# Optimization experiments

Hardware: AMD Instinct MI355X
Metric: run time of the kernel (lower is better)

Reference implementation:

```python
import jax, jax.numpy as jnp
import numpy as np

N_NODES = 50000
N_EDGES = 800000
IN_DIM = 128
HIDDEN = 128
OUT_DIM = 128


def setup_inputs() -> dict:
    key = jax.random.key(0)
    ks = jax.random.split(key, 16)
    s = 0.05
    inp = {
        "x": jax.random.normal(ks[0], (N_NODES, IN_DIM), jnp.float32),
        "edge_index": jax.random.randint(ks[1], (2, N_EDGES), 0, N_NODES, jnp.int64),
        "batch": jax.random.randint(ks[2], (25000,), 0, N_NODES, jnp.int64),
        "labels": jax.random.randint(ks[3], (N_NODES,), 0, 2, jnp.int64),
        # SAGEConv layer 1: in->hidden
        "W1l": jax.random.normal(ks[4], (HIDDEN, IN_DIM), jnp.float32) * s,
        "b1": jnp.zeros((HIDDEN,), jnp.float32),
        "W1r": jax.random.normal(ks[5], (HIDDEN, IN_DIM), jnp.float32) * s,
        # SAGEConv layer 2: hidden->hidden
        "W2l": jax.random.normal(ks[6], (HIDDEN, HIDDEN), jnp.float32) * s,
        "b2": jnp.zeros((HIDDEN,), jnp.float32),
        "W2r": jax.random.normal(ks[7], (HIDDEN, HIDDEN), jnp.float32) * s,
        # SAGEConv layer 3: hidden->out
        "W3l": jax.random.normal(ks[8], (OUT_DIM, HIDDEN), jnp.float32) * s,
        "b3": jnp.zeros((OUT_DIM,), jnp.float32),
        "W3r": jax.random.normal(ks[9], (OUT_DIM, HIDDEN), jnp.float32) * s,
        # classifier head: out->2
        "Wlin": jax.random.normal(ks[10], (2, OUT_DIM), jnp.float32) * s,
        "blin": jnp.zeros((2,), jnp.float32),
    }
    return inp


def _sage_conv(h, src, dst, Wl, bl, Wr):
    # mean aggregation of source features at destination nodes
    msg = h[src]                                            # [E, d]
    ssum = jax.ops.segment_sum(msg, dst, num_segments=N_NODES)
    cnt = jax.ops.segment_sum(jnp.ones((src.shape[0], 1), h.dtype), dst,
                              num_segments=N_NODES)
    agg = ssum / jnp.maximum(cnt, 1.0)
    # lin_l(agg) + lin_r(h): aggregate-then-transform (same math, cheaper)
    return agg @ Wl.T + bl + h @ Wr.T


def reference(x, edge_index, batch, labels,
              W1l, b1, W1r, W2l, b2, W2r, W3l, b3, W3r, Wlin, blin):
    src, dst = edge_index[0], edge_index[1]
    h = jax.nn.relu(_sage_conv(x, src, dst, W1l, b1, W1r))
    h = jax.nn.relu(_sage_conv(h, src, dst, W2l, b2, W2r))
    h = _sage_conv(h, src, dst, W3l, b3, W3r)               # no act after last
    preds = jax.nn.softmax(h @ Wlin.T + blin, axis=1)       # nn.Softmax(dim=1)
    # CrossEntropyLoss on (already-softmaxed) preds, as in the original module
    logp = jax.nn.log_softmax(preds[batch], axis=1)
    loss = -jnp.mean(jnp.take_along_axis(logp, labels[batch][:, None], axis=1))
    return loss
```

## Files before the change

### kernel.cpp

```cpp
#include <hip/hip_runtime.h>
#include <hip/hip_bf16.h>

#define N_NODES 50000
#define MPAD    50048
#define N_EDGES 800000
#define DIM     128
#define N_BATCH 25000
#define NBUCK   196
#define BCAP    8192
#define NBIN    64

typedef unsigned short u16;
typedef unsigned int   u32;
typedef unsigned char  u8;
typedef unsigned long long u64;

typedef __attribute__((ext_vector_type(8))) short bf16x8;
typedef __attribute__((ext_vector_type(4))) float f32x4;

static __device__ __forceinline__ float bf2f(u16 u) {
    union { u32 i; float f; } v; v.i = ((u32)u) << 16; return v.f;
}
static __device__ __forceinline__ u16 f2bf(float f) {
    union { float f; u32 i; } v; v.f = f;
    u32 x = v.i;
    u32 r = x + 0x7fffu + ((x >> 16) & 1u);
    return (u16)(r >> 16);
}


__global__ void k_init(int* bcur, float* accum, int* hcount,
                       u8* mask, int* h1g, int* h3g) {
    int gid = blockIdx.x * 256 + threadIdx.x;
    if (gid < NBUCK) bcur[gid] = gid * BCAP;
    if (gid < NBIN) { h1g[gid] = 0; h3g[gid] = 0; }
    if (gid < N_NODES) mask[gid] = 0;
    if (gid == 0) { accum[0] = 0.f; hcount[0] = 0; }
}

__global__ void k_mark(const int* __restrict__ batch, u8* __restrict__ mask) {
    int s = blockIdx.x * 256 + threadIdx.x;
    if (s < N_BATCH) mask[batch[s]] = 1;
}


__global__ __launch_bounds__(256) void k_part(const int* __restrict__ src,
                                              const int* __restrict__ dst,
                                              int* __restrict__ bcur,
                                              u64* __restrict__ ebuf) {
    __shared__ int hist[NBUCK];
    __shared__ int lbase[NBUCK];
    __shared__ int gdelta[NBUCK];
    __shared__ u64 stage[4096];
    __shared__ int gaddr[4096];
    int t = threadIdx.x;
    for (int i = t; i < NBUCK; i += 256) hist[i] = 0;
    __syncthreads();

    int base = blockIdx.x * 4096;
    int cnt = N_EDGES - base; if (cnt > 4096) cnt = 4096; if (cnt < 0) cnt = 0;

    int es[16], ed[16], rr[16];
#pragma unroll
    for (int k = 0; k < 16; ++k) {
        int i = t + (k << 8);
        bool ok = i < cnt;
        int e = ok ? (base + i) : 0;
        int s = src[e], d = dst[e];
        es[k] = s; ed[k] = d;
        int r = -1;
        if (ok) r = atomicAdd(&hist[d >> 8], 1);
        rr[k] = r;
    }
    __syncthreads();

    if (t < 64) {
        int run = 0;
        for (int c = 0; c < 4; ++c) {
            int idx = c * 64 + t;
            int v = (idx < NBUCK) ? hist[idx] : 0;
            int orig = v;
            for (int off = 1; off < 64; off <<= 1) {
                int u = __shfl_up(v, off);
                if (t >= off) v += u;
            }
            int tot = __shfl(v, 63);
            if (idx < NBUCK) lbase[idx] = run + v - orig;
            run += tot;
        }
    }
    __syncthreads();

    if (t < NBUCK) {
        int c = hist[t];
        int g = atomicAdd(&bcur[t], c);
        gdelta[t] = g - lbase[t];
    }
    __syncthreads();

#pragma unroll
    for (int k = 0; k < 16; ++k) {
        if (rr[k] >= 0) {
            int b = ed[k] >> 8;
            int slot = lbase[b] + rr[k];
            stage[slot] = (((u64)(u32)ed[k]) << 32) | (u32)es[k];
            gaddr[slot] = gdelta[b] + slot;
        }
    }
    __syncthreads();

    for (int i = t; i < cnt; i += 256) {
        ebuf[gaddr[i]] = stage[i];
    }
}


__global__ void k_bscan(const int* __restrict__ bcur, int* __restrict__ bbase) {
    int t = threadIdx.x;
    int run = 0;
    for (int c = 0; c < 4; ++c) {
        int idx = c * 64 + t;
        int v = (idx < NBUCK) ? (bcur[idx] - idx * BCAP) : 0;
        int orig = v;
        for (int off = 1; off < 64; off <<= 1) {
            int u = __shfl_up(v, off);
            if (t >= off) v += u;
        }
        int tot = __shfl(v, 63);
        if (idx < NBUCK) bbase[idx] = run + v - orig;
        run += tot;
    }
}


__global__ __launch_bounds__(256) void k_build(const u64* __restrict__ ebuf,
                                               const int* __restrict__ bcur,
                                               const int* __restrict__ bbase,
                                               const u8* __restrict__ mask,
                                               int* __restrict__ row_ptr,
                                               int* __restrict__ deg,
                                               float* __restrict__ deg_inv,
                                               int* __restrict__ csr_src,
                                               int* __restrict__ h1g,
                                               int* __restrict__ h3g) {
    __shared__ int cnt256[256];
    __shared__ int sh[256];
    __shared__ int cur[256];
    __shared__ int bh1[NBIN];
    __shared__ int bh3[NBIN];
    int b  = blockIdx.x;
    int t  = threadIdx.x;
    int n0 = b << 8;
    cnt256[t] = 0;
    if (t < NBIN) { bh1[t] = 0; bh3[t] = 0; }
    __syncthreads();

    int cnt = bcur[b] - b * BCAP;
    const u64* eb = ebuf + (size_t)b * BCAP;
    for (int i = t; i < cnt; i += 256) {
        int d = (int)(eb[i] >> 32);
        atomicAdd(&cnt256[d - n0], 1);
    }
    __syncthreads();

    int myc = cnt256[t];
    sh[t] = myc;
    __syncthreads();
    for (int off = 1; off < 256; off <<= 1) {
        int x = (t >= off) ? sh[t - off] : 0;
        __syncthreads();
        sh[t] += x;
        __syncthreads();
    }
    int rp = bbase[b] + sh[t] - myc;
    int n  = n0 + t;
    if (n < N_NODES) {
        row_ptr[n] = rp;
        deg[n]     = myc;
        deg_inv[n] = 1.0f / (float)(myc < 1 ? 1 : myc);
        int bin = myc < NBIN ? myc : NBIN - 1;
        atomicAdd(&bh1[bin], 1);
        if (mask[n]) atomicAdd(&bh3[bin], 1);
    }
    cur[t] = rp;
    __syncthreads();

    for (int i = t; i < cnt; i += 256) {
        u64 p = eb[i];
        int d = (int)(p >> 32);
        int s = (int)(u32)p;
        int pos = atomicAdd(&cur[d - n0], 1);
        csr_src[pos] = s;
    }
    __syncthreads();
    if (t < NBIN) {
        if (bh1[t]) atomicAdd(&h1g[t], bh1[t]);
        if (bh3[t]) atomicAdd(&h3g[t], bh3[t]);
    }
}


__global__ void k_dscan(int* __restrict__ h1g, int* __restrict__ h3g,
                        int* __restrict__ n3out) {
    int t = threadIdx.x;
    int v1 = h1g[t], v3 = h3g[t];
    int o1 = v1, o3 = v3;
    for (int off = 1; off < 64; off <<= 1) {
        int u1 = __shfl_up(v1, off);
        int u3 = __shfl_up(v3, off);
        if (t >= off) { v1 += u1; v3 += u3; }
    }
    if (t == 63) n3out[0] = v3;
    h1g[t] = v1 - o1;
    h3g[t] = v3 - o3;
}


__global__ __launch_bounds__(256) void k_dscatter(const int* __restrict__ deg,
                                                  const u8* __restrict__ mask,
                                                  int* __restrict__ h1g,
                                                  int* __restrict__ h3g,
                                                  int* __restrict__ wl1,
                                                  int* __restrict__ wl3) {
    __shared__ int bh1[NBIN], bh3[NBIN], bb1[NBIN], bb3[NBIN];
    int t = threadIdx.x;
    int n = blockIdx.x * 256 + t;
    if (t < NBIN) { bh1[t] = 0; bh3[t] = 0; }
    __syncthreads();
    bool valid = n < N_NODES;
    int d = 0, r1 = -1, r3 = -1;
    if (valid) {
        d = deg[n]; if (d >= NBIN) d = NBIN - 1;
        r1 = atomicAdd(&bh1[d], 1);
        if (mask[n]) r3 = atomicAdd(&bh3[d], 1);
    }
    __syncthreads();
    if (t < NBIN) {
        bb1[t] = atomicAdd(&h1g[t], bh1[t]);
        bb3[t] = atomicAdd(&h3g[t], bh3[t]);
    }
    __syncthreads();
    if (valid) {
        wl1[bb1[d] + r1] = n;
        if (r3 >= 0) wl3[bb3[d] + r3] = n;
    }
}


__global__ void k_cast_x(const float* __restrict__ x, u16* __restrict__ xb) {
    int gid = blockIdx.x * 256 + threadIdx.x;
    int row = gid >> 4;
    int c8  = (gid & 15) << 3;
    u32 outw[4];
    if (row < N_NODES) {
        const float4* p = (const float4*)(x + (size_t)row * DIM + c8);
        float4 v0 = p[0], v1 = p[1];
        outw[0] = (u32)f2bf(v0.x) | ((u32)f2bf(v0.y) << 16);
        outw[1] = (u32)f2bf(v0.z) | ((u32)f2bf(v0.w) << 16);
        outw[2] = (u32)f2bf(v1.x) | ((u32)f2bf(v1.y) << 16);
        outw[3] = (u32)f2bf(v1.z) | ((u32)f2bf(v1.w) << 16);
    } else {
        outw[0] = outw[1] = outw[2] = outw[3] = 0;
    }
    *(uint4*)(xb + (size_t)row * DIM + c8) = *(uint4*)outw;
}

__global__ void k_cast_w(const float* __restrict__ W1l, const float* __restrict__ W1r,
                         const float* __restrict__ W2l, const float* __restrict__ W2r,
                         const float* __restrict__ W3l, const float* __restrict__ W3r,
                         u16* __restrict__ out) {
    int i = blockIdx.x * 256 + threadIdx.x;
    int mat = i >> 14, off = i & 16383;
    const float* src = (mat == 0) ? W1l : (mat == 1) ? W1r : (mat == 2) ? W2l
                     : (mat == 3) ? W2r : (mat == 4) ? W3l : W3r;
    out[i] = f2bf(src[off]);
}


template <bool RELU, bool PRUNED>
__global__ __launch_bounds__(256) void k_sage(
    const u16* __restrict__ h, const int* __restrict__ csr_src,
    const int* __restrict__ row_ptr, const int* __restrict__ deg,
    const float* __restrict__ deg_inv,
    const int* __restrict__ wl, const int* __restrict__ wlN,
    const u16* __restrict__ Wl, const u16* __restrict__ Wr,
    const float* __restrict__ bias, u16* __restrict__ out) {
    __shared__ u16 tile[16 * 128];
    __shared__ int wlid[16];
    int nwl = PRUNED ? wlN[0] : N_NODES;
    int m0  = blockIdx.x * 16;
    if (m0 >= nwl) return;

    int t    = threadIdx.x;
    int lane = t & 63;
    int wid  = t >> 6;
    int sub  = lane & 15;
    int grp  = lane >> 4;
    int nloc = (wid << 2) + grp;
    int gb   = lane & 48;
    int node = (m0 + nloc < nwl) ? wl[m0 + nloc] : -1;
    if (sub == 0) wlid[nloc] = node;

    float a0 = 0, a1 = 0, a2 = 0, a3 = 0, a4 = 0, a5 = 0, a6 = 0, a7 = 0;

#define ACC(u) { a0 += bf2f((u16)((u).x & 0xffffu)); a1 += bf2f((u16)((u).x >> 16)); \
                 a2 += bf2f((u16)((u).y & 0xffffu)); a3 += bf2f((u16)((u).y >> 16)); \
                 a4 += bf2f((u16)((u).z & 0xffffu)); a5 += bf2f((u16)((u).z >> 16)); \
                 a6 += bf2f((u16)((u).w & 0xffffu)); a7 += bf2f((u16)((u).w >> 16)); }

    if (node >= 0) {
        int start = row_ptr[node];
        int cnt   = deg[node];
        for (int c0 = 0; c0 < cnt; c0 += 16) {
            int rem = cnt - c0; if (rem > 16) rem = 16;
            int sidx = 0;
            if (sub < rem) sidx = csr_src[start + c0 + sub];
            int j = 0;
            for (; j + 8 <= rem; j += 8) {
                int i0 = __shfl(sidx, gb + j);
                int i1 = __shfl(sidx, gb + j + 1);
                int i2 = __shfl(sidx, gb + j + 2);
                int i3 = __shfl(sidx, gb + j + 3);
                int i4 = __shfl(sidx, gb + j + 4);
                int i5 = __shfl(sidx, gb + j + 5);
                int i6 = __shfl(sidx, gb + j + 6);
                int i7 = __shfl(sidx, gb + j + 7);
                uint4 r0 = *(const uint4*)(h + (size_t)i0 * DIM + sub * 8);
                uint4 r1 = *(const uint4*)(h + (size_t)i1 * DIM + sub * 8);
                uint4 r2 = *(const uint4*)(h + (size_t)i2 * DIM + sub * 8);
                uint4 r3 = *(const uint4*)(h + (size_t)i3 * DIM + sub * 8);
                uint4 r4 = *(const uint4*)(h + (size_t)i4 * DIM + sub * 8);
                uint4 r5 = *(const uint4*)(h + (size_t)i5 * DIM + sub * 8);
                uint4 r6 = *(const uint4*)(h + (size_t)i6 * DIM + sub * 8);
                uint4 r7 = *(const uint4*)(h + (size_t)i7 * DIM + sub * 8);
                ACC(r0); ACC(r1); ACC(r2); ACC(r3);
                ACC(r4); ACC(r5); ACC(r6); ACC(r7);
            }
            for (; j + 4 <= rem; j += 4) {
                int i0 = __shfl(sidx, gb + j);
                int i1 = __shfl(sidx, gb + j + 1);
                int i2 = __shfl(sidx, gb + j + 2);
                int i3 = __shfl(sidx, gb + j + 3);
                uint4 r0 = *(const uint4*)(h + (size_t)i0 * DIM + sub * 8);
                uint4 r1 = *(const uint4*)(h + (size_t)i1 * DIM + sub * 8);
                uint4 r2 = *(const uint4*)(h + (size_t)i2 * DIM + sub * 8);
                uint4 r3 = *(const uint4*)(h + (size_t)i3 * DIM + sub * 8);
                ACC(r0); ACC(r1); ACC(r2); ACC(r3);
            }
            for (; j < rem; ++j) {
                int i0 = __shfl(sidx, gb + j);
                uint4 r0 = *(const uint4*)(h + (size_t)i0 * DIM + sub * 8);
                ACC(r0);
            }
        }
        float inv = deg_inv[node];
        a0 *= inv; a1 *= inv; a2 *= inv; a3 *= inv;
        a4 *= inv; a5 *= inv; a6 *= inv; a7 *= inv;
    }
#undef ACC

    {
        uint4 o;
        o.x = (u32)f2bf(a0) | ((u32)f2bf(a1) << 16);
        o.y = (u32)f2bf(a2) | ((u32)f2bf(a3) << 16);
        o.z = (u32)f2bf(a4) | ((u32)f2bf(a5) << 16);
        o.w = (u32)f2bf(a6) | ((u32)f2bf(a7) << 16);
        int chunk = sub ^ (nloc & 7);
        *(uint4*)&tile[nloc * 128 + chunk * 8] = o;
    }
    __syncthreads();

    const int fr = sub;
    const int kq = grp << 3;
    bf16x8 aF0[4], aF1[4];
    int rnode = wlid[fr];
    int safe_r = rnode < 0 ? 0 : rnode;
    const u16* ph = h + (size_t)safe_r * DIM + kq;
#pragma unroll
    for (int kt = 0; kt < 4; ++kt) {
        int c = (grp + kt * 4) ^ (fr & 7);
        aF0[kt] = *(const bf16x8*)&tile[fr * 128 + c * 8];
        aF1[kt] = *(const bf16x8*)(ph + kt * 32);
    }
#pragma unroll
    for (int q = 0; q < 2; ++q) {
        int nt = wid * 2 + q;
        const u16* pwl = Wl + (size_t)(nt * 16 + fr) * DIM + kq;
        const u16* pwr = Wr + (size_t)(nt * 16 + fr) * DIM + kq;
        f32x4 acc = {0.f, 0.f, 0.f, 0.f};
#pragma unroll
        for (int kt = 0; kt < 4; ++kt) {
            bf16x8 w = *(const bf16x8*)(pwl + kt * 32);
            acc = __builtin_amdgcn_mfma_f32_16x16x32_bf16(aF0[kt], w, acc, 0, 0, 0);
        }
#pragma unroll
        for (int kt = 0; kt < 4; ++kt) {
            bf16x8 w = *(const bf16x8*)(pwr + kt * 32);
            acc = __builtin_amdgcn_mfma_f32_16x16x32_bf16(aF1[kt], w, acc, 0, 0, 0);
        }
        int col = nt * 16 + fr;
        float b = bias[col];
#pragma unroll
        for (int j = 0; j < 4; ++j) {
            int onode = wlid[(grp << 2) + j];
            if (onode >= 0) {
                float v = acc[j] + b;
                if (RELU) v = fmaxf(v, 0.f);
                out[(size_t)onode * DIM + col] = f2bf(v);
            }
        }
    }
}


__global__ __launch_bounds__(256) void k_head(
    const u16* __restrict__ h3, const int* __restrict__ batch,
    const int* __restrict__ labels, const float* __restrict__ Wlin,
    const float* __restrict__ blin, float* __restrict__ accum,
    int* __restrict__ hcount, float* __restrict__ out) {
    __shared__ float wsh[256];
    __shared__ float red[4];
    int t = threadIdx.x;
    wsh[t] = Wlin[t];
    __syncthreads();

    int lane = t & 63;
    int g    = lane >> 4;
    int sub  = lane & 15;
    int wv   = (blockIdx.x * 256 + t) >> 6;
    int samp = wv * 4 + g;

    float contrib = 0.f;
    float z0 = 0.f, z1 = 0.f;
    int n = 0;
    if (samp < N_BATCH) {
        n = batch[samp];
        uint4 u = *(const uint4*)(h3 + (size_t)n * DIM + sub * 8);
        const u32* uw = (const u32*)&u;
        int cb = sub * 8;
#pragma unroll
        for (int q = 0; q < 4; ++q) {
            float hlo = bf2f((u16)(uw[q] & 0xffffu));
            float hhi = bf2f((u16)(uw[q] >> 16));
            z0 += hlo * wsh[cb + q * 2]       + hhi * wsh[cb + q * 2 + 1];
            z1 += hlo * wsh[128 + cb + q * 2] + hhi * wsh[128 + cb + q * 2 + 1];
        }
    }
#pragma unroll
    for (int off = 8; off > 0; off >>= 1) {
        z0 += __shfl_xor(z0, off);
        z1 += __shfl_xor(z1, off);
    }
    if (samp < N_BATCH) {
        z0 += blin[0]; z1 += blin[1];
        float m  = fmaxf(z0, z1);
        float e0 = expf(z0 - m), e1 = expf(z1 - m);
        float s  = e0 + e1;
        float p0 = e0 / s, p1 = e1 / s;
        float m2  = fmaxf(p0, p1);
        float lse = m2 + logf(expf(p0 - m2) + expf(p1 - m2));
        int lab = labels[n];
        float lp = ((lab == 0) ? p0 : p1) - lse;
        if (sub == 0) contrib = -lp * (1.0f / (float)N_BATCH);
    }
#pragma unroll
    for (int off = 16; off < 64; off <<= 1) contrib += __shfl_xor(contrib, off);
    if (lane == 0) red[t >> 6] = contrib;
    __syncthreads();
    if (t == 0) {
        atomicAdd(accum, red[0] + red[1] + red[2] + red[3]);
        __threadfence();
        int c = atomicAdd(hcount, 1);
        if (c == (int)gridDim.x - 1) {
            float v = atomicAdd(accum, 0.0f);
            out[0] = v;
        }
    }
}


extern "C" void kernel_launch(void* const* d_in, const int* in_sizes, int n_in,
                              void* d_out, int out_size, void* d_ws, size_t ws_size,
                              hipStream_t stream) {
    const float* x    = (const float*)d_in[0];
    const int*   eidx = (const int*)d_in[1];
    const int*   batch  = (const int*)d_in[2];
    const int*   labels = (const int*)d_in[3];
    const float* W1l = (const float*)d_in[4];
    const float* b1  = (const float*)d_in[5];
    const float* W1r = (const float*)d_in[6];
    const float* W2l = (const float*)d_in[7];
    const float* b2  = (const float*)d_in[8];
    const float* W2r = (const float*)d_in[9];
    const float* W3l = (const float*)d_in[10];
    const float* b3  = (const float*)d_in[11];
    const float* W3r = (const float*)d_in[12];
    const float* Wlin = (const float*)d_in[13];
    const float* blin = (const float*)d_in[14];

    const int* src = eidx;
    const int* dst = eidx + N_EDGES;

    size_t off = 0;
    auto alloc = [&](size_t bytes) -> char* {
        off = (off + 511) & ~(size_t)511;
        char* p = (char*)d_ws + off;
        off += bytes;
        return p;
    };
    int*   bcur    = (int*)  alloc(NBUCK * 4);
    int*   bbase   = (int*)  alloc(NBUCK * 4);
    int*   row_ptr = (int*)  alloc(N_NODES * 4);
    int*   deg     = (int*)  alloc(N_NODES * 4);
    float* deg_inv = (float*)alloc(N_NODES * 4);
    int*   csr_src = (int*)  alloc(N_EDGES * 4);
    u64*   ebuf    = (u64*)  alloc((size_t)NBUCK * BCAP * 8);
    u16*   wb      = (u16*)  alloc(6 * DIM * DIM * 2);
    u16*   xb      = (u16*)  alloc((size_t)MPAD * DIM * 2);
    u16*   bufA    = (u16*)  alloc((size_t)MPAD * DIM * 2);
    u8*    mask    = (u8*)   alloc(N_NODES);
    int*   h1g     = (int*)  alloc(NBIN * 4);
    int*   h3g     = (int*)  alloc(NBIN * 4);
    int*   wl1     = (int*)  alloc(MPAD * 4);
    int*   wl3     = (int*)  alloc(MPAD * 4);
    int*   n3      = (int*)  alloc(4);
    float* accum   = (float*)alloc(4);
    int*   hcount  = (int*)  alloc(4);

    u16* bufB = xb;

    u16* w1l = wb + 0 * DIM * DIM;
    u16* w1r = wb + 1 * DIM * DIM;
    u16* w2l = wb + 2 * DIM * DIM;
    u16* w2r = wb + 3 * DIM * DIM;
    u16* w3l = wb + 4 * DIM * DIM;
    u16* w3r = wb + 5 * DIM * DIM;

    const int NB196 = (N_NODES + 255) / 256;
    const int PB    = (N_EDGES + 4095) / 4096;
    const int MB    = (N_BATCH + 255) / 256;
    const int CXB   = MPAD * 16 / 256;
    const int CWB   = 6 * DIM * DIM / 256;
    const int SGB   = N_NODES / 16;
    const int HB2   = (N_BATCH + 15) / 16;

    k_init<<<NB196, 256, 0, stream>>>(bcur, accum, hcount, mask, h1g, h3g);
    k_part<<<PB, 256, 0, stream>>>(src, dst, bcur, ebuf);
    k_bscan<<<1, 64, 0, stream>>>(bcur, bbase);
    k_mark<<<MB, 256, 0, stream>>>(batch, mask);
    k_build<<<NBUCK, 256, 0, stream>>>(ebuf, bcur, bbase, mask, row_ptr, deg,
                                       deg_inv, csr_src, h1g, h3g);
    k_dscan<<<1, 64, 0, stream>>>(h1g, h3g, n3);
    k_dscatter<<<NB196, 256, 0, stream>>>(deg, mask, h1g, h3g, wl1, wl3);

    k_cast_x<<<CXB, 256, 0, stream>>>(x, xb);
    k_cast_w<<<CWB, 256, 0, stream>>>(W1l, W1r, W2l, W2r, W3l, W3r, wb);

    k_sage<true, false><<<SGB, 256, 0, stream>>>(xb, csr_src, row_ptr, deg, deg_inv,
                                                 wl1, n3, w1l, w1r, b1, bufA);
    k_sage<true, false><<<SGB, 256, 0, stream>>>(bufA, csr_src, row_ptr, deg, deg_inv,
                                                 wl1, n3, w2l, w2r, b2, bufB);
    k_sage<false, true><<<SGB, 256, 0, stream>>>(bufB, csr_src, row_ptr, deg, deg_inv,
                                                 wl3, n3, w3l, w3r, b3, bufA);

    k_head<<<HB2, 256, 0, stream>>>(bufA, batch, labels, Wlin, blin,
                                    accum, hcount, (float*)d_out);
}
```

Before: 218.7 us.

## Gather neighbor features in FP8 and fuse setup kernels to cut launches

Measured after the change: 191.1 us (median of 2 runs). -12.6%, faster.

```diff
diff --git a/kernel.cpp b/kernel.cpp
--- a/kernel.cpp
+++ b/kernel.cpp
@@ -17,6 +17,7 @@
 
 typedef __attribute__((ext_vector_type(8))) short bf16x8;
 typedef __attribute__((ext_vector_type(4))) float f32x4;
+typedef __attribute__((ext_vector_type(2))) float f32x2;
 
 static __device__ __forceinline__ float bf2f(u16 u) {
     union { u32 i; float f; } v; v.i = ((u32)u) << 16; return v.f;
@@ -27,133 +28,166 @@
     u32 r = x + 0x7fffu + ((x >> 16) & 1u);
     return (u16)(r >> 16);
 }
-
-
-__global__ void k_init(int* bcur, float* accum, int* hcount,
-                       u8* mask, int* h1g, int* h3g) {
+template <bool HI>
+static __device__ __forceinline__ u32 pk8(float a, float b, u32 old) {
+    return (u32)__builtin_amdgcn_cvt_pk_fp8_f32(a, b, (int)old, HI);
+}
+
+
+__global__ void k_init(int* bcur, float* accum, int* hcount, u8* mask,
+                       int* c1g, int* c3g, int* o1g, int* o3g) {
     int gid = blockIdx.x * 256 + threadIdx.x;
     if (gid < NBUCK) bcur[gid] = gid * BCAP;
-    if (gid < NBIN) { h1g[gid] = 0; h3g[gid] = 0; }
+    if (gid < NBIN) { c1g[gid] = 0; c3g[gid] = 0; o1g[gid] = 0; o3g[gid] = 0; }
     if (gid < N_NODES) mask[gid] = 0;
     if (gid == 0) { accum[0] = 0.f; hcount[0] = 0; }
 }
 
-__global__ void k_mark(const int* __restrict__ batch, u8* __restrict__ mask) {
-    int s = blockIdx.x * 256 + threadIdx.x;
-    if (s < N_BATCH) mask[batch[s]] = 1;
-}
-
-
-__global__ __launch_bounds__(256) void k_part(const int* __restrict__ src,
-                                              const int* __restrict__ dst,
-                                              int* __restrict__ bcur,
-                                              u64* __restrict__ ebuf) {
+
+#define SB_PART 196
+#define SB_CX   3324
+#define SB_CW   3708
+#define SB_MK   3806
+
+__global__ __launch_bounds__(256) void k_setup(
+    const int* __restrict__ src, const int* __restrict__ dst,
+    int* __restrict__ bcur, u64* __restrict__ ebuf,
+    const float* __restrict__ x, u16* __restrict__ xb, u8* __restrict__ x8,
+    const float* __restrict__ W1l, const float* __restrict__ W1r,
+    const float* __restrict__ W2l, const float* __restrict__ W2r,
+    const float* __restrict__ W3l, const float* __restrict__ W3r,
+    u16* __restrict__ wout,
+    const int* __restrict__ batch, u8* __restrict__ mask) {
     __shared__ int hist[NBUCK];
     __shared__ int lbase[NBUCK];
     __shared__ int gdelta[NBUCK];
     __shared__ u64 stage[4096];
     __shared__ int gaddr[4096];
+    int bid = blockIdx.x;
     int t = threadIdx.x;
-    for (int i = t; i < NBUCK; i += 256) hist[i] = 0;
-    __syncthreads();
-
-    int base = blockIdx.x * 4096;
-    int cnt = N_EDGES - base; if (cnt > 4096) cnt = 4096; if (cnt < 0) cnt = 0;
-
-    int es[16], ed[16], rr[16];
-#pragma unroll
-    for (int k = 0; k < 16; ++k) {
-        int i = t + (k << 8);
-        bool ok = i < cnt;
-        int e = ok ? (base + i) : 0;
-        int s = src[e], d = dst[e];
-        es[k] = s; ed[k] = d;
-        int r = -1;
-        if (ok) r = atomicAdd(&hist[d >> 8], 1);
-        rr[k] = r;
-    }
-    __syncthreads();
-
-    if (t < 64) {
-        int run = 0;
-        for (int c = 0; c < 4; ++c) {
-            int idx = c * 64 + t;
-            int v = (idx < NBUCK) ? hist[idx] : 0;
-            int orig = v;
-            for (int off = 1; off < 64; off <<= 1) {
-                int u = __shfl_up(v, off);
-                if (t >= off) v += u;
+
+    if (bid < SB_PART) {
+        for (int i = t; i < NBUCK; i += 256) hist[i] = 0;
+        __syncthreads();
+
+        int base = bid * 4096;
+        int cnt = N_EDGES - base; if (cnt > 4096) cnt = 4096; if (cnt < 0) cnt = 0;
+
+        int es[16], ed[16], rr[16];
+#pragma unroll
+        for (int k = 0; k < 16; ++k) {
+            int i = t + (k << 8);
+            bool ok = i < cnt;
+            int e = ok ? (base + i) : 0;
+            int s = src[e], d = dst[e];
+            es[k] = s; ed[k] = d;
+            int r = -1;
+            if (ok) r = atomicAdd(&hist[d >> 8], 1);
+            rr[k] = r;
+        }
+        __syncthreads();
+
+        if (t < 64) {
+            int run = 0;
+            for (int c = 0; c < 4; ++c) {
+                int idx = c * 64 + t;
+                int v = (idx < NBUCK) ? hist[idx] : 0;
+                int orig = v;
+                for (int off = 1; off < 64; off <<= 1) {
+                    int u = __shfl_up(v, off);
+                    if (t >= off) v += u;
+                }
+                int tot = __shfl(v, 63);
+                if (idx < NBUCK) lbase[idx] = run + v - orig;
+                run += tot;
             }
-            int tot = __shfl(v, 63);
-            if (idx < NBUCK) lbase[idx] = run + v - orig;
-            run += tot;
-        }
-    }
-    __syncthreads();
-
-    if (t < NBUCK) {
-        int c = hist[t];
-        int g = atomicAdd(&bcur[t], c);
-        gdelta[t] = g - lbase[t];
-    }
-    __syncthreads();
-
-#pragma unroll
-    for (int k = 0; k < 16; ++k) {
-        if (rr[k] >= 0) {
-            int b = ed[k] >> 8;
-            int slot = lbase[b] + rr[k];
-            stage[slot] = (((u64)(u32)ed[k]) << 32) | (u32)es[k];
-            gaddr[slot] = gdelta[b] + slot;
-        }
-    }
-    __syncthreads();
-
-    for (int i = t; i < cnt; i += 256) {
-        ebuf[gaddr[i]] = stage[i];
-    }
-}
-
-
-__global__ void k_bscan(const int* __restrict__ bcur, int* __restrict__ bbase) {
-    int t = threadIdx.x;
-    int run = 0;
-    for (int c = 0; c < 4; ++c) {
-        int idx = c * 64 + t;
-        int v = (idx < NBUCK) ? (bcur[idx] - idx * BCAP) : 0;
-        int orig = v;
-        for (int off = 1; off < 64; off <<= 1) {
-            int u = __shfl_up(v, off);
-            if (t >= off) v += u;
-        }
-        int tot = __shfl(v, 63);
-        if (idx < NBUCK) bbase[idx] = run + v - orig;
-        run += tot;
+        }
+        __syncthreads();
+
+        if (t < NBUCK) {
+            int c = hist[t];
+            int g = atomicAdd(&bcur[t], c);
+            gdelta[t] = g - lbase[t];
+        }
+        __syncthreads();
+
+#pragma unroll
+        for (int k = 0; k < 16; ++k) {
+            if (rr[k] >= 0) {
+                int b = ed[k] >> 8;
+                int slot = lbase[b] + rr[k];
+                stage[slot] = (((u64)(u32)ed[k]) << 32) | (u32)es[k];
+                gaddr[slot] = gdelta[b] + slot;
+            }
+        }
+        __syncthreads();
+
+        for (int i = t; i < cnt; i += 256) {
+            ebuf[gaddr[i]] = stage[i];
+        }
+    } else if (bid < SB_CX) {
+        int gid = (bid - SB_PART) * 256 + t;
+        int row = gid >> 4;
+        int c8  = (gid & 15) << 3;
+        u32 outw[4];
+        u32 w0 = 0, w1 = 0;
+        if (row < N_NODES) {
+            const float4* p = (const float4*)(x + (size_t)row * DIM + c8);
+            float4 v0 = p[0], v1 = p[1];
+            outw[0] = (u32)f2bf(v0.x) | ((u32)f2bf(v0.y) << 16);
+            outw[1] = (u32)f2bf(v0.z) | ((u32)f2bf(v0.w) << 16);
+            outw[2] = (u32)f2bf(v1.x) | ((u32)f2bf(v1.y) << 16);
+            outw[3] = (u32)f2bf(v1.z) | ((u32)f2bf(v1.w) << 16);
+            w0 = pk8<false>(v0.x, v0.y, 0); w0 = pk8<true>(v0.z, v0.w, w0);
+            w1 = pk8<false>(v1.x, v1.y, 0); w1 = pk8<true>(v1.z, v1.w, w1);
+        } else {
+            outw[0] = outw[1] = outw[2] = outw[3] = 0;
+        }
+        *(uint4*)(xb + (size_t)row * DIM + c8) = *(uint4*)outw;
+        uint2 o8; o8.x = w0; o8.y = w1;
+        *(uint2*)(x8 + (size_t)row * DIM + c8) = o8;
+    } else if (bid < SB_CW) {
+        int i = (bid - SB_CX) * 256 + t;
+        int mat = i >> 14, off = i & 16383;
+        const float* s = (mat == 0) ? W1l : (mat == 1) ? W1r : (mat == 2) ? W2l
+                       : (mat == 3) ? W2r : (mat == 4) ? W3l : W3r;
+        wout[i] = f2bf(s[off]);
+    } else {
+        int s = (bid - SB_CW) * 256 + t;
+        if (s < N_BATCH) mask[batch[s]] = 1;
     }
 }
 
 
 __global__ __launch_bounds__(256) void k_build(const u64* __restrict__ ebuf,
                                                const int* __restrict__ bcur,
-                                               const int* __restrict__ bbase,
                                                const u8* __restrict__ mask,
                                                int* __restrict__ row_ptr,
                                                int* __restrict__ deg,
                                                float* __restrict__ deg_inv,
                                                int* __restrict__ csr_src,
-                                               int* __restrict__ h1g,
-                                               int* __restrict__ h3g) {
+                                               int* __restrict__ c1g,
+                                               int* __restrict__ c3g) {
     __shared__ int cnt256[256];
     __shared__ int sh[256];
     __shared__ int cur[256];
     __shared__ int bh1[NBIN];
     __shared__ int bh3[NBIN];
+    __shared__ int shbase;
     int b  = blockIdx.x;
     int t  = threadIdx.x;
     int n0 = b << 8;
     cnt256[t] = 0;
     if (t < NBIN) { bh1[t] = 0; bh3[t] = 0; }
-    __syncthreads();
+    if (t < 64) {
+        int s = 0;
+        for (int i = t; i < b; i += 64) s += bcur[i] - i * BCAP;
+#pragma unroll
+        for (int off = 32; off > 0; off >>= 1) s += __shfl_xor(s, off);
+        if (t == 0) shbase = s;
+    }
+    __syncthreads();
+    int bbase = shbase;
 
     int cnt = bcur[b] - b * BCAP;
     const u64* eb = ebuf + (size_t)b * BCAP;
@@ -172,7 +206,7 @@
         sh[t] += x;
         __syncthreads();
     }
-    int rp = bbase[b] + sh[t] - myc;
+    int rp = bbase + sh[t] - myc;
     int n  = n0 + t;
     if (n < N_NODES) {
         row_ptr[n] = rp;
@@ -194,34 +228,21 @@
     }
     __syncthreads();
     if (t < NBIN) {
-        if (bh1[t]) atomicAdd(&h1g[t], bh1[t]);
-        if (bh3[t]) atomicAdd(&h3g[t], bh3[t]);
-    }
-}
-
-
-__global__ void k_dscan(int* __restrict__ h1g, int* __restrict__ h3g,
-                        int* __restrict__ n3out) {
-    int t = threadIdx.x;
-    int v1 = h1g[t], v3 = h3g[t];
-    int o1 = v1, o3 = v3;
-    for (int off = 1; off < 64; off <<= 1) {
-        int u1 = __shfl_up(v1, off);
-        int u3 = __shfl_up(v3, off);
-        if (t >= off) { v1 += u1; v3 += u3; }
-    }
-    if (t == 63) n3out[0] = v3;
-    h1g[t] = v1 - o1;
-    h3g[t] = v3 - o3;
+        if (bh1[t]) atomicAdd(&c1g[t], bh1[t]);
+        if (bh3[t]) atomicAdd(&c3g[t], bh3[t]);
+    }
 }
 
 
 __global__ __launch_bounds__(256) void k_dscatter(const int* __restrict__ deg,
                                                   const u8* __restrict__ mask,
-                                                  int* __restrict__ h1g,
-                                                  int* __restrict__ h3g,
+                                                  const int* __restrict__ c1g,
+                                                  const int* __restrict__ c3g,
+                                                  int* __restrict__ o1g,
+                                                  int* __restrict__ o3g,
                                                   int* __restrict__ wl1,
-                                                  int* __restrict__ wl3) {
+                                                  int* __restrict__ wl3,
+                                                  int* __restrict__ n3) {
     __shared__ int bh1[NBIN], bh3[NBIN], bb1[NBIN], bb3[NBIN];
     int t = threadIdx.x;
     int n = blockIdx.x * 256 + t;
@@ -235,9 +256,19 @@
         if (mask[n]) r3 = atomicAdd(&bh3[d], 1);
     }
     __syncthreads();
-    if (t < NBIN) {
-        bb1[t] = atomicAdd(&h1g[t], bh1[t]);
-        bb3[t] = atomicAdd(&h3g[t], bh3[t]);
+    if (t < 64) {
+        int v1 = c1g[t], v3 = c3g[t];
+        int i1 = v1, i3 = v3;
+        for (int off = 1; off < 64; off <<= 1) {
+            int u1 = __shfl_up(i1, off);
+            int u3 = __shfl_up(i3, off);
+            if (t >= off) { i1 += u1; i3 += u3; }
+        }
+        int res1 = atomicAdd(&o1g[t], bh1[t]);
+        int res3 = atomicAdd(&o3g[t], bh3[t]);
+        bb1[t] = (i1 - v1) + res1;
+        bb3[t] = (i3 - v3) + res3;
+        if (blockIdx.x == 0 && t == 63) n3[0] = i3;
     }
     __syncthreads();
     if (valid) {
@@ -247,44 +278,16 @@
 }
 
 
-__global__ void k_cast_x(const float* __restrict__ x, u16* __restrict__ xb) {
-    int gid = blockIdx.x * 256 + threadIdx.x;
-    int row = gid >> 4;
-    int c8  = (gid & 15) << 3;
-    u32 outw[4];
-    if (row < N_NODES) {
-        const float4* p = (const float4*)(x + (size_t)row * DIM + c8);
-        float4 v0 = p[0], v1 = p[1];
-        outw[0] = (u32)f2bf(v0.x) | ((u32)f2bf(v0.y) << 16);
-        outw[1] = (u32)f2bf(v0.z) | ((u32)f2bf(v0.w) << 16);
-        outw[2] = (u32)f2bf(v1.x) | ((u32)f2bf(v1.y) << 16);
-        outw[3] = (u32)f2bf(v1.z) | ((u32)f2bf(v1.w) << 16);
-    } else {
-        outw[0] = outw[1] = outw[2] = outw[3] = 0;
-    }
-    *(uint4*)(xb + (size_t)row * DIM + c8) = *(uint4*)outw;
-}
-
-__global__ void k_cast_w(const float* __restrict__ W1l, const float* __restrict__ W1r,
-                         const float* __restrict__ W2l, const float* __restrict__ W2r,
-                         const float* __restrict__ W3l, const float* __restrict__ W3r,
-                         u16* __restrict__ out) {
-    int i = blockIdx.x * 256 + threadIdx.x;
-    int mat = i >> 14, off = i & 16383;
-    const float* src = (mat == 0) ? W1l : (mat == 1) ? W1r : (mat == 2) ? W2l
-                     : (mat == 3) ? W2r : (mat == 4) ? W3l : W3r;
-    out[i] = f2bf(src[off]);
-}
-
-
-template <bool RELU, bool PRUNED>
+template <bool RELU, bool PRUNED, bool W8>
 __global__ __launch_bounds__(256) void k_sage(
-    const u16* __restrict__ h, const int* __restrict__ csr_src,
+    const u16* __restrict__ h, const u8* __restrict__ h8,
+    const int* __restrict__ csr_src,
     const int* __restrict__ row_ptr, const int* __restrict__ deg,
     const float* __restrict__ deg_inv,
     const int* __restrict__ wl, const int* __restrict__ wlN,
     const u16* __restrict__ Wl, const u16* __restrict__ Wr,
-    const float* __restrict__ bias, u16* __restrict__ out) {
+    const float* __restrict__ bias, u16* __restrict__ out,
+    u8* __restrict__ out8) {
     __shared__ u16 tile[16 * 128];
     __shared__ int wlid[16];
     int nwl = PRUNED ? wlN[0] : N_NODES;
@@ -303,10 +306,11 @@
 
     float a0 = 0, a1 = 0, a2 = 0, a3 = 0, a4 = 0, a5 = 0, a6 = 0, a7 = 0;
 
-#define ACC(u) { a0 += bf2f((u16)((u).x & 0xffffu)); a1 += bf2f((u16)((u).x >> 16)); \
-                 a2 += bf2f((u16)((u).y & 0xffffu)); a3 += bf2f((u16)((u).y >> 16)); \
-                 a4 += bf2f((u16)((u).z & 0xffffu)); a5 += bf2f((u16)((u).z >> 16)); \
-                 a6 += bf2f((u16)((u).w & 0xffffu)); a7 += bf2f((u16)((u).w >> 16)); }
+#define ACC8(r) { f32x2 p; \
+    p = __builtin_amdgcn_cvt_pk_f32_fp8((r).x, false); a0 += p[0]; a1 += p[1]; \
+    p = __builtin_amdgcn_cvt_pk_f32_fp8((r).x, true);  a2 += p[0]; a3 += p[1]; \
+    p = __builtin_amdgcn_cvt_pk_f32_fp8((r).y, false); a4 += p[0]; a5 += p[1]; \
+    p = __builtin_amdgcn_cvt_pk_f32_fp8((r).y, true);  a6 += p[0]; a7 += p[1]; }
 
     if (node >= 0) {
         int start = row_ptr[node];
@@ -325,39 +329,39 @@
                 int i5 = __shfl(sidx, gb + j + 5);
                 int i6 = __shfl(sidx, gb + j + 6);
                 int i7 = __shfl(sidx, gb + j + 7);
-                uint4 r0 = *(const uint4*)(h + (size_t)i0 * DIM + sub * 8);
-                uint4 r1 = *(const uint4*)(h + (size_t)i1 * DIM + sub * 8);
-                uint4 r2 = *(const uint4*)(h + (size_t)i2 * DIM + sub * 8);
-                uint4 r3 = *(const uint4*)(h + (size_t)i3 * DIM + sub * 8);
-                uint4 r4 = *(const uint4*)(h + (size_t)i4 * DIM + sub * 8);
-                uint4 r5 = *(const uint4*)(h + (size_t)i5 * DIM + sub * 8);
-                uint4 r6 = *(const uint4*)(h + (size_t)i6 * DIM + sub * 8);
-                uint4 r7 = *(const uint4*)(h + (size_t)i7 * DIM + sub * 8);
-                ACC(r0); ACC(r1); ACC(r2); ACC(r3);
-                ACC(r4); ACC(r5); ACC(r6); ACC(r7);
+                uint2 r0 = *(const uint2*)(h8 + (size_t)i0 * DIM + sub * 8);
+                uint2 r1 = *(const uint2*)(h8 + (size_t)i1 * DIM + sub * 8);
+                uint2 r2 = *(const uint2*)(h8 + (size_t)i2 * DIM + sub * 8);
+                uint2 r3 = *(const uint2*)(h8 + (size_t)i3 * DIM + sub * 8);
+                uint2 r4 = *(const uint2*)(h8 + (size_t)i4 * DIM + sub * 8);
+                uint2 r5 = *(const uint2*)(h8 + (size_t)i5 * DIM + sub * 8);
+                uint2 r6 = *(const uint2*)(h8 + (size_t)i6 * DIM + sub * 8);
+                uint2 r7 = *(const uint2*)(h8 + (size_t)i7 * DIM + sub * 8);
+                ACC8(r0); ACC8(r1); ACC8(r2); ACC8(r3);
+                ACC8(r4); ACC8(r5); ACC8(r6); ACC8(r7);
             }
             for (; j + 4 <= rem; j += 4) {
                 int i0 = __shfl(sidx, gb + j);
                 int i1 = __shfl(sidx, gb + j + 1);
                 int i2 = __shfl(sidx, gb + j + 2);
                 int i3 = __shfl(sidx, gb + j + 3);
-                uint4 r0 = *(const uint4*)(h + (size_t)i0 * DIM + sub * 8);
-                uint4 r1 = *(const uint4*)(h + (size_t)i1 * DIM + sub * 8);
-                uint4 r2 = *(const uint4*)(h + (size_t)i2 * DIM + sub * 8);
-                uint4 r3 = *(const uint4*)(h + (size_t)i3 * DIM + sub * 8);
-                ACC(r0); ACC(r1); ACC(r2); ACC(r3);
+                uint2 r0 = *(const uint2*)(h8 + (size_t)i0 * DIM + sub * 8);
+                uint2 r1 = *(const uint2*)(h8 + (size_t)i1 * DIM + sub * 8);
+                uint2 r2 = *(const uint2*)(h8 + (size_t)i2 * DIM + sub * 8);
+                uint2 r3 = *(const uint2*)(h8 + (size_t)i3 * DIM + sub * 8);
+                ACC8(r0); ACC8(r1); ACC8(r2); ACC8(r3);
             }
             for (; j < rem; ++j) {
                 int i0 = __shfl(sidx, gb + j);
-                uint4 r0 = *(const uint4*)(h + (size_t)i0 * DIM + sub * 8);
-                ACC(r0);
+                uint2 r0 = *(const uint2*)(h8 + (size_t)i0 * DIM + sub * 8);
+                ACC8(r0);
             }
         }
         float inv = deg_inv[node];
         a0 *= inv; a1 *= inv; a2 *= inv; a3 *= inv;
         a4 *= inv; a5 *= inv; a6 *= inv; a7 *= inv;
     }
-#undef ACC
+#undef ACC8
 
     {
         uint4 o;
@@ -407,6 +411,7 @@
                 float v = acc[j] + b;
                 if (RELU) v = fmaxf(v, 0.f);
                 out[(size_t)onode * DIM + col] = f2bf(v);
+                if (W8) out8[(size_t)onode * DIM + col] = (u8)(pk8<false>(v, v, 0) & 0xffu);
             }
         }
     }
@@ -509,7 +514,6 @@
         return p;
     };
     int*   bcur    = (int*)  alloc(NBUCK * 4);
-    int*   bbase   = (int*)  alloc(NBUCK * 4);
     int*   row_ptr = (int*)  alloc(N_NODES * 4);
     int*   deg     = (int*)  alloc(N_NODES * 4);
     float* deg_inv = (float*)alloc(N_NODES * 4);
@@ -518,9 +522,14 @@
     u16*   wb      = (u16*)  alloc(6 * DIM * DIM * 2);
     u16*   xb      = (u16*)  alloc((size_t)MPAD * DIM * 2);
     u16*   bufA    = (u16*)  alloc((size_t)MPAD * DIM * 2);
+    u8*    x8      = (u8*)   alloc((size_t)MPAD * DIM);
+    u8*    a8      = (u8*)   alloc((size_t)MPAD * DIM);
+    u8*    b8      = (u8*)   alloc((size_t)MPAD * DIM);
     u8*    mask    = (u8*)   alloc(N_NODES);
-    int*   h1g     = (int*)  alloc(NBIN * 4);
-    int*   h3g     = (int*)  alloc(NBIN * 4);
+    int*   c1g     = (int*)  alloc(NBIN * 4);
+    int*   c3g     = (int*)  alloc(NBIN * 4);
+    int*   o1g     = (int*)  alloc(NBIN * 4);
+    int*   o3g     = (int*)  alloc(NBIN * 4);
     int*   wl1     = (int*)  alloc(MPAD * 4);
     int*   wl3     = (int*)  alloc(MPAD * 4);
     int*   n3      = (int*)  alloc(4);
@@ -537,31 +546,25 @@
     u16* w3r = wb + 5 * DIM * DIM;
 
     const int NB196 = (N_NODES + 255) / 256;
-    const int PB    = (N_EDGES + 4095) / 4096;
-    const int MB    = (N_BATCH + 255) / 256;
-    const int CXB   = MPAD * 16 / 256;
-    const int CWB   = 6 * DIM * DIM / 256;
     const int SGB   = N_NODES / 16;
     const int HB2   = (N_BATCH + 15) / 16;
 
-    k_init<<<NB196, 256, 0, stream>>>(bcur, accum, hcount, mask, h1g, h3g);
-    k_part<<<PB, 256, 0, stream>>>(src, dst, bcur, ebuf);
-    k_bscan<<<1, 64, 0, stream>>>(bcur, bbase);
-    k_mark<<<MB, 256, 0, stream>>>(batch, mask);
-    k_build<<<NBUCK, 256, 0, stream>>>(ebuf, bcur, bbase, mask, row_ptr, deg,
-                                       deg_inv, csr_src, h1g, h3g);
-    k_dscan<<<1, 64, 0, stream>>>(h1g, h3g, n3);
-    k_dscatter<<<NB196, 256, 0, stream>>>(deg, mask, h1g, h3g, wl1, wl3);
-
-    k_cast_x<<<CXB, 256, 0, stream>>>(x, xb);
-    k_cast_w<<<CWB, 256, 0, stream>>>(W1l, W1r, W2l, W2r, W3l, W3r, wb);
-
-    k_sage<true, false><<<SGB, 256, 0, stream>>>(xb, csr_src, row_ptr, deg, deg_inv,
-                                                 wl1, n3, w1l, w1r, b1, bufA);
-    k_sage<true, false><<<SGB, 256, 0, stream>>>(bufA, csr_src, row_ptr, deg, deg_inv,
-                                                 wl1, n3, w2l, w2r, b2, bufB);
-    k_sage<false, true><<<SGB, 256, 0, stream>>>(bufB, csr_src, row_ptr, deg, deg_inv,
-                                                 wl3, n3, w3l, w3r, b3, bufA);
+    k_init<<<NB196, 256, 0, stream>>>(bcur, accum, hcount, mask, c1g, c3g, o1g, o3g);
+    k_setup<<<SB_MK, 256, 0, stream>>>(src, dst, bcur, ebuf,
+                                       x, xb, x8,
+                                       W1l, W1r, W2l, W2r, W3l, W3r, wb,
+                                       batch, mask);
+    k_build<<<NBUCK, 256, 0, stream>>>(ebuf, bcur, mask, row_ptr, deg,
+                                       deg_inv, csr_src, c1g, c3g);
+    k_dscatter<<<NB196, 256, 0, stream>>>(deg, mask, c1g, c3g, o1g, o3g,
+                                          wl1, wl3, n3);
+
+    k_sage<true, false, true><<<SGB, 256, 0, stream>>>(
+        xb, x8, csr_src, row_ptr, deg, deg_inv, wl1, n3, w1l, w1r, b1, bufA, a8);
+    k_sage<true, false, true><<<SGB, 256, 0, stream>>>(
+        bufA, a8, csr_src, row_ptr, deg, deg_inv, wl1, n3, w2l, w2r, b2, bufB, b8);
+    k_sage<false, true, false><<<SGB, 256, 0, stream>>>(
+        bufB, b8, csr_src, row_ptr, deg, deg_inv, wl3, n3, w3l, w3r, b3, bufA, nullptr);
 
     k_head<<<HB2, 256, 0, stream>>>(bufA, batch, labels, Wlin, blin,
                                     accum, hcount, (float*)d_out);
```
